# Kernel optimization log

Hardware: AMD Instinct MI355X
Metric: run time of the kernel (lower is better)

Reference implementation:

```python
import jax, jax.numpy as jnp
import numpy as np
from jax import lax

N_LAYERS = 4
D_MODEL = 256
D_INNER = 512   # expand * d_model
D_STATE = 16
D_CONV = 4
DT_RANK = 16    # ceil(d_model/16)
N_FEATURES = 32
N_CLASSES = 3
BATCH, SEQ = 8, 2048


def _layernorm(x, w, b, eps=1e-5):
    mu = x.mean(-1, keepdims=True)
    var = ((x - mu) ** 2).mean(-1, keepdims=True)
    return (x - mu) * lax.rsqrt(var + eps) * w + b


def _silu(x):
    return x * jax.nn.sigmoid(x)


def _ssm(xc, xpW, dtW, dtB, A_log, D):
    # xc: (B,S,d_inner)
    xd = xc @ xpW                                    # (B,S,dt_rank+2*d_state)
    dt_r = xd[..., :DT_RANK]
    Bm = xd[..., DT_RANK:DT_RANK + D_STATE]          # (B,S,N)
    Cm = xd[..., DT_RANK + D_STATE:]                 # (B,S,N)
    dt = jax.nn.softplus(dt_r @ dtW + dtB)           # (B,S,d_inner)
    A = -jnp.exp(A_log)                              # (d_inner,N)
    dA = jnp.exp(dt[..., None] * A)                  # (B,S,d_inner,N)
    dBx = dt[..., None] * Bm[:, :, None, :] * xc[..., None]  # (B,S,d_inner,N)

    def step(h, inp):
        dA_t, dBx_t, C_t = inp                       # (B,d_inner,N),(B,d_inner,N),(B,N)
        h = dA_t * h + dBx_t
        y_t = (h * C_t[:, None, :]).sum(-1)          # (B,d_inner)
        return h, y_t

    h0 = jnp.zeros((xc.shape[0], D_INNER, D_STATE), xc.dtype)
    xs = (dA.transpose(1, 0, 2, 3), dBx.transpose(1, 0, 2, 3), Cm.transpose(1, 0, 2))
    _, ys = lax.scan(step, h0, xs)                   # (S,B,d_inner)
    y = ys.transpose(1, 0, 2)
    return y + xc * D


def _mamba_block(x, inW, convW, convB, xpW, dtW, dtB, A_log, D, outW):
    xz = x @ inW                                     # (B,S,2*d_inner)
    xs, z = xz[..., :D_INNER], xz[..., D_INNER:]
    # causal depthwise conv1d (left-pad d_conv-1)
    xp = jnp.pad(xs, ((0, 0), (D_CONV - 1, 0), (0, 0)))
    xc = lax.conv_general_dilated(
        xp, convW, window_strides=(1,), padding='VALID',
        dimension_numbers=('NWC', 'WIO', 'NWC'),
        feature_group_count=D_INNER) + convB
    xc = _silu(xc)
    y = _ssm(xc, xpW, dtW, dtB, A_log, D)
    y = y * _silu(z)
    return y @ outW


def setup_inputs() -> dict:
    key = jax.random.key(0)
    ks = jax.random.split(key, 20)
    s = 0.02
    L = N_LAYERS
    inp = {
        'x': jax.random.normal(ks[0], (BATCH, SEQ, N_FEATURES), jnp.float32),
        'in_w': jax.random.normal(ks[1], (N_FEATURES, D_MODEL), jnp.float32) * s,
        'in_b': jnp.zeros((D_MODEL,), jnp.float32),
        'ln_w': jnp.ones((L, D_MODEL), jnp.float32),
        'ln_b': jnp.zeros((L, D_MODEL), jnp.float32),
        'inW': jax.random.normal(ks[2], (L, D_MODEL, 2 * D_INNER), jnp.float32) * s,
        'convW': jax.random.normal(ks[3], (L, D_CONV, 1, D_INNER), jnp.float32) * s,
        'convB': jnp.zeros((L, D_INNER), jnp.float32),
        'xpW': jax.random.normal(ks[4], (L, D_INNER, DT_RANK + 2 * D_STATE), jnp.float32) * s,
        'dtW': jax.random.uniform(ks[5], (L, DT_RANK, D_INNER), jnp.float32,
                                  -DT_RANK ** -0.5, DT_RANK ** -0.5),
        'A_log': jnp.broadcast_to(jnp.log(jnp.arange(1, D_STATE + 1, dtype=jnp.float32)),
                                  (L, D_INNER, D_STATE)).copy(),
        'D': jnp.ones((L, D_INNER), jnp.float32),
        'outW': jax.random.normal(ks[6], (L, D_INNER, D_MODEL), jnp.float32) * s,
        'fln_w': jnp.ones((D_MODEL,), jnp.float32),
        'fln_b': jnp.zeros((D_MODEL,), jnp.float32),
        'h1W': jax.random.normal(ks[7], (D_MODEL, D_MODEL // 2), jnp.float32) * s,
        'h1b': jnp.zeros((D_MODEL // 2,), jnp.float32),
        'h2W': jax.random.normal(ks[8], (D_MODEL // 2, N_CLASSES), jnp.float32) * s,
        'h2b': jnp.zeros((N_CLASSES,), jnp.float32),
    }
    # dt bias init: inv softplus of dt ~ LogUniform(dt_min, dt_max)
    dt_min, dt_max = 1e-3, 0.1
    u = jax.random.uniform(ks[9], (L, D_INNER), jnp.float32)
    dt = jnp.clip(jnp.exp(u * (np.log(dt_max) - np.log(dt_min)) + np.log(dt_min)), 1e-4)
    inp['dtB'] = dt + jnp.log(-jnp.expm1(-dt))
    return inp


def reference(x, in_w, in_b, ln_w, ln_b, inW, convW, convB, xpW, dtW, dtB,
              A_log, D, outW, fln_w, fln_b, h1W, h1b, h2W, h2b):
    h = x @ in_w + in_b                              # (B,S,d_model); dropout is eval-mode identity
    for i in range(N_LAYERS):
        h = h + _mamba_block(_layernorm(h, ln_w[i], ln_b[i]),
                             inW[i], convW[i], convB[i], xpW[i],
                             dtW[i], dtB[i], A_log[i], D[i], outW[i])
    h = _layernorm(h, fln_w, fln_b)
    last = h[:, -1]                                  # (B,d_model)
    hidden = jax.nn.gelu(last @ h1W + h1b)
    return hidden @ h2W + h2b                        # (B,n_classes)
```

## Files before the change

kernel.cpp:

```cpp
#include <hip/hip_runtime.h>
#include <math.h>

namespace {

constexpr int NL = 4;
constexpr int DM = 256;
constexpr int DI = 512;
constexpr int DS = 16;
constexpr int DR = 16;
constexpr int NF = 32;
constexpr int NB = 8;
constexpr int T  = 2048;
constexpr int ROWS = NB * T;
constexpr int XD = DR + 2 * DS;
constexpr int NC = 64;
constexpr int CL = T / NC;
constexpr int SCN = NB * DI * DS;

constexpr float LOG2E = 1.44269504088896341f;
constexpr float LN2   = 0.69314718055994531f;

typedef __attribute__((ext_vector_type(4))) float f32x4;
typedef __attribute__((ext_vector_type(8))) short bf16x8;
typedef __attribute__((ext_vector_type(4))) short s16x4;

__device__ __forceinline__ float fexp2(float x) { return __builtin_amdgcn_exp2f(x); }
__device__ __forceinline__ float frcp(float x)  { return __builtin_amdgcn_rcpf(x); }
__device__ __forceinline__ float flog2(float x) { return __builtin_amdgcn_logf(x); }

__device__ __forceinline__ float siluf(float x) {
    return x * frcp(1.f + fexp2(-LOG2E * x));
}
__device__ __forceinline__ float softplusf(float x) {
    return fmaxf(x, 0.f) + LN2 * flog2(1.f + fexp2(-LOG2E * fabsf(x)));
}
__device__ __forceinline__ short f2bf(float f) {
    union { float f; unsigned u; } c; c.f = f;
    unsigned r = (c.u + 0x7FFFu + ((c.u >> 16) & 1u)) >> 16;
    return (short)r;
}
__device__ __forceinline__ float bf2f(short s) {
    union { unsigned u; float f; } c; c.u = ((unsigned)(unsigned short)s) << 16;
    return c.f;
}
__device__ __forceinline__ void powers16(float g, float* a) {
    float g2 = g * g, g4 = g2 * g2, g8 = g4 * g4;
    a[0] = g;        a[1] = g2;       a[2] = g * g2;   a[3] = g4;
    a[4] = g * g4;   a[5] = g2 * g4;  a[6] = a[2] * g4; a[7] = g8;
    a[8] = g * g8;   a[9] = g2 * g8;  a[10] = a[2] * g8; a[11] = g4 * g8;
    a[12] = a[4] * g8; a[13] = a[5] * g8; a[14] = a[6] * g8; a[15] = g8 * g8;
}

__global__ void wtrans(const float* __restrict__ src, short* __restrict__ dst,
                       int K, int N, int Npad, int perL_dst)
{
    const int idx = blockIdx.x * 256 + threadIdx.x;
    const int l = idx / perL_dst;
    const int r = idx - l * perL_dst;
    const unsigned n = (unsigned)r / (unsigned)K;
    const unsigned k = (unsigned)r - n * (unsigned)K;
    float v = (n < (unsigned)N) ? src[(size_t)l * K * N + k * N + n] : 0.f;
    dst[idx] = f2bf(v);
}

__global__ void prep_dtWt(const float* __restrict__ dtW, float* __restrict__ dtWt)
{
    const int idx = blockIdx.x * 256 + threadIdx.x;
    const int l = idx / (DI * DR);
    const int r0 = idx - l * (DI * DR);
    const int d = r0 / DR, rr = r0 - d * DR;
    dtWt[idx] = dtW[(size_t)l * DR * DI + rr * DI + d];
}

__global__ void prep_A2(const float* __restrict__ A_log, float* __restrict__ negA2)
{
    const int i = blockIdx.x * 256 + threadIdx.x;
    negA2[i] = -LOG2E * fexp2(LOG2E * A_log[i]);
}

__global__ void cvt_bf16(const float* __restrict__ src, short* __restrict__ dst)
{
    const int i = blockIdx.x * 256 + threadIdx.x;
    dst[i] = f2bf(src[i]);
}

template <int EP, int BM>
__global__ void gemm_mfma(const short* __restrict__ A, const short* __restrict__ Bt,
                          float* __restrict__ C, short* __restrict__ Cs0,
                          short* __restrict__ Cs1, const float* __restrict__ bias,
                          int K, int lda, int ldc, int Ncut, int NXB, int NYB)
{
    constexpr int MF = BM / 32;
    __shared__ short smem[BM * 40 + 64 * 40];
    const int bid = blockIdx.x;
    const int xcd = bid & 7, j = bid >> 3;
    const int by = xcd * (NYB >> 3) + j / NXB;
    const int bx = j - (j / NXB) * NXB;
    const int m0 = by * BM;
    const int n0 = bx * 64;

    const int tid = threadIdx.x;
    const int lane = tid & 63, w = tid >> 6;
    const int wr = w >> 1, wc = w & 1;
    const int lr = lane & 15, lk = lane >> 4;

    f32x4 acc[MF][2] = {};
    for (int k0 = 0; k0 < K; k0 += 32) {
        __syncthreads();
#pragma unroll
        for (int i = 0; i < BM / 64; ++i) {
            int c = tid + i * 256;
            int row = c >> 2, seg = c & 3;
            bf16x8 v = *(const bf16x8*)(A + (size_t)(m0 + row) * lda + k0 + seg * 8);
            *(bf16x8*)(&smem[row * 40 + seg * 8]) = v;
        }
        {
            int row = tid >> 2, seg = tid & 3;
            bf16x8 v = *(const bf16x8*)(Bt + (size_t)(n0 + row) * K + k0 + seg * 8);
            *(bf16x8*)(&smem[BM * 40 + row * 40 + seg * 8]) = v;
        }
        __syncthreads();
        bf16x8 af[MF], bfr[2];
#pragma unroll
        for (int m = 0; m < MF; ++m)
            af[m] = *(const bf16x8*)(&smem[(wr * (BM / 2) + m * 16 + lr) * 40 + lk * 8]);
#pragma unroll
        for (int n = 0; n < 2; ++n)
            bfr[n] = *(const bf16x8*)(&smem[BM * 40 + (wc * 32 + n * 16 + lr) * 40 + lk * 8]);
#pragma unroll
        for (int m = 0; m < MF; ++m)
#pragma unroll
            for (int n = 0; n < 2; ++n)
                acc[m][n] = __builtin_amdgcn_mfma_f32_16x16x32_bf16(af[m], bfr[n], acc[m][n], 0, 0, 0);
    }
#pragma unroll
    for (int m = 0; m < MF; ++m) {
#pragma unroll
        for (int n = 0; n < 2; ++n) {
            const int col = n0 + wc * 32 + n * 16 + lr;
#pragma unroll
            for (int j2 = 0; j2 < 4; ++j2) {
                const int row = m0 + wr * (BM / 2) + m * 16 + lk * 4 + j2;
                const float v = acc[m][n][j2];
                if (EP == 0) {
                    if (col < DI) Cs0[(size_t)row * DI + col] = f2bf(v);
                    else          Cs1[(size_t)row * DI + col - DI] = f2bf(siluf(v));
                } else if (EP == 1) {
                    if (col < Ncut) C[(size_t)row * ldc + col] = v;
                } else if (EP == 2) {
                    C[(size_t)row * ldc + col] += v;
                } else {
                    C[(size_t)row * ldc + col] = v + bias[col];
                }
            }
        }
    }
}

__global__ void layernorm_kernel(const float* __restrict__ x,
                                 const float* __restrict__ w,
                                 const float* __restrict__ b,
                                 short* __restrict__ out)
{
    const int row = blockIdx.x;
    const int t = threadIdx.x;
    const int wid = t >> 6, lane = t & 63;
    __shared__ float red[4];

    float v = x[row * DM + t];
    float s = v;
#pragma unroll
    for (int o = 32; o >= 1; o >>= 1) s += __shfl_xor(s, o);
    if (lane == 0) red[wid] = s;
    __syncthreads();
    float mu = (red[0] + red[1] + red[2] + red[3]) * (1.f / DM);
    __syncthreads();

    float d = v - mu;
    float q = d * d;
#pragma unroll
    for (int o = 32; o >= 1; o >>= 1) q += __shfl_xor(q, o);
    if (lane == 0) red[wid] = q;
    __syncthreads();
    float var = (red[0] + red[1] + red[2] + red[3]) * (1.f / DM);

    out[row * DM + t] = f2bf(d * (1.f / sqrtf(var + 1e-5f)) * w[t] + b[t]);
}

__global__ void conv_silu_kernel(const short* __restrict__ xsb,
                                 const float* __restrict__ W,
                                 const float* __restrict__ Bc,
                                 short* __restrict__ xcb)
{
    const int idx = blockIdx.x * 256 + threadIdx.x;
    const int c4 = idx & (DI / 4 - 1);
    const int bt = idx >> 7;
    const int t = bt & (T - 1);
    const int c = c4 * 4;
    f32x4 acc = *(const f32x4*)(Bc + c);
#pragma unroll
    for (int k = 0; k < 4; ++k) {
        int tt = t + k - 3;
        if (tt >= 0) {
            s16x4 v = *(const s16x4*)(xsb + (size_t)(bt + k - 3) * DI + c);
            f32x4 wv = *(const f32x4*)(W + k * DI + c);
#pragma unroll
            for (int q = 0; q < 4; ++q) acc[q] += bf2f(v[q]) * wv[q];
        }
    }
    s16x4 o;
#pragma unroll
    for (int q = 0; q < 4; ++q) o[q] = f2bf(siluf(acc[q]));
    *(s16x4*)(xcb + (size_t)idx * 4) = o;
}

__global__ void scan_pass1(const float* __restrict__ xd,
                           const short* __restrict__ xcb,
                           const float* __restrict__ negA2,
                           const float* __restrict__ dtWt,
                           const float* __restrict__ dtB,
                           float* __restrict__ S, float* __restrict__ sdtb)
{
    __shared__ float lds[CL][32];
    const int d = blockIdx.x * 256 + threadIdx.x;
    const int c = blockIdx.y;
    const int b = blockIdx.z;
    const int row0 = b * T + c * CL;

    {
        int t = threadIdx.x >> 3, seg = threadIdx.x & 7;
        *(f32x4*)&lds[t][seg * 4] =
            *(const f32x4*)(xd + (size_t)(row0 + t) * XD + seg * 4);
    }
    float A2[DS], h[DS], wcol[DR];
#pragma unroll
    for (int q = 0; q < 4; ++q) {
        *(f32x4*)&A2[q * 4]   = *(const f32x4*)(negA2 + d * DS + q * 4);
        *(f32x4*)&wcol[q * 4] = *(const f32x4*)(dtWt + d * DR + q * 4);
    }
    bool fastb = true;
#pragma unroll
    for (int s = 1; s < DS; ++s)
        fastb = fastb && (fabsf(A2[s] - A2[0] * (float)(s + 1)) <= 1e-4f * fabsf(A2[s]));
    const bool fast = __all(fastb);
#pragma unroll
    for (int s = 0; s < DS; ++s) h[s] = 0.f;
    const float dtBd = dtB[d];
    float sdt = 0.f;
    __syncthreads();

    for (int t = 0; t < CL; ++t) {
        float xcv = bf2f(xcb[(size_t)(row0 + t) * DI + d]);
        float accd = dtBd;
#pragma unroll
        for (int q = 0; q < 4; ++q) {
            f32x4 xr = *(const f32x4*)&lds[t][q * 4];
            accd += xr[0] * wcol[q * 4] + xr[1] * wcol[q * 4 + 1]
                  + xr[2] * wcol[q * 4 + 2] + xr[3] * wcol[q * 4 + 3];
        }
        float dtv = softplusf(accd);
        float dx = dtv * xcv;
        sdt += dtv;
        float a[DS];
        if (fast) powers16(fexp2(dtv * A2[0]), a);
        else {
#pragma unroll
            for (int s = 0; s < DS; ++s) a[s] = fexp2(dtv * A2[s]);
        }
#pragma unroll
        for (int q = 0; q < 4; ++q) {
            f32x4 Bv = *(const f32x4*)&lds[t][16 + q * 4];
#pragma unroll
            for (int s = 0; s < 4; ++s)
                h[q * 4 + s] = a[q * 4 + s] * h[q * 4 + s] + dx * Bv[s];
        }
    }
    const size_t base = (size_t)c * SCN + ((size_t)b * DI + d) * DS;
#pragma unroll
    for (int q = 0; q < 4; ++q)
        *(f32x4*)(S + base + q * 4) = *(f32x4*)&h[q * 4];
    sdtb[c * (NB * DI) + b * DI + d] = sdt;
}

__global__ void scan_combine(float* __restrict__ S, const float* __restrict__ sdtb,
                             const float* __restrict__ negA2)
{
    const int idx3 = blockIdx.x * blockDim.x + threadIdx.x;
    const int bd = idx3 >> 4;
    const float A2c = negA2[(bd & (DI - 1)) * DS + (idx3 & 15)];
    float h = 0.f;
    for (int c = 0; c < NC; ++c) {
        float sc = S[(size_t)c * SCN + idx3];
        float pc = fexp2(A2c * sdtb[c * (NB * DI) + bd]);
        S[(size_t)c * SCN + idx3] = h;
        h = pc * h + sc;
    }
}

__global__ void scan_pass2(const float* __restrict__ xd,
                           const short* __restrict__ xcb,
                           const float* __restrict__ negA2,
                           const float* __restrict__ dtWt,
                           const float* __restrict__ dtB,
                           const float* __restrict__ Dv,
                           const float* __restrict__ H,
                           const short* __restrict__ zgb,
                           short* __restrict__ yb)
{
    __shared__ float lds[CL][48];
    const int d = blockIdx.x * 256 + threadIdx.x;
    const int c = blockIdx.y;
    const int b = blockIdx.z;
    const int row0 = b * T + c * CL;

    for (int c0 = threadIdx.x; c0 < CL * 12; c0 += 256) {
        int t = c0 / 12, seg = c0 - t * 12;
        *(f32x4*)&lds[t][seg * 4] =
            *(const f32x4*)(xd + (size_t)(row0 + t) * XD + seg * 4);
    }
    float A2[DS], h[DS], wcol[DR];
#pragma unroll
    for (int q = 0; q < 4; ++q) {
        *(f32x4*)&A2[q * 4]   = *(const f32x4*)(negA2 + d * DS + q * 4);
        *(f32x4*)&wcol[q * 4] = *(const f32x4*)(dtWt + d * DR + q * 4);
    }
    bool fastb = true;
#pragma unroll
    for (int s = 1; s < DS; ++s)
        fastb = fastb && (fabsf(A2[s] - A2[0] * (float)(s + 1)) <= 1e-4f * fabsf(A2[s]));
    const bool fast = __all(fastb);
    const size_t base = (size_t)c * SCN + ((size_t)b * DI + d) * DS;
#pragma unroll
    for (int q = 0; q < 4; ++q)
        *(f32x4*)&h[q * 4] = *(const f32x4*)(H + base + q * 4);
    const float dtBd = dtB[d];
    const float Dd = Dv[d];
    __syncthreads();

    for (int t = 0; t < CL; ++t) {
        const size_t row = (size_t)(row0 + t);
        float xcv = bf2f(xcb[row * DI + d]);
        float zg  = bf2f(zgb[row * DI + d]);
        float accd = dtBd;
#pragma unroll
        for (int q = 0; q < 4; ++q) {
            f32x4 xr = *(const f32x4*)&lds[t][q * 4];
            accd += xr[0] * wcol[q * 4] + xr[1] * wcol[q * 4 + 1]
                  + xr[2] * wcol[q * 4 + 2] + xr[3] * wcol[q * 4 + 3];
        }
        float dtv = softplusf(accd);
        float dx = dtv * xcv;
        float a[DS];
        if (fast) powers16(fexp2(dtv * A2[0]), a);
        else {
#pragma unroll
            for (int s = 0; s < DS; ++s) a[s] = fexp2(dtv * A2[s]);
        }
        float acc0 = 0.f, acc1 = 0.f, acc2 = 0.f, acc3 = 0.f;
#pragma unroll
        for (int q = 0; q < 4; ++q) {
            f32x4 Bv = *(const f32x4*)&lds[t][16 + q * 4];
            f32x4 Cv = *(const f32x4*)&lds[t][32 + q * 4];
            h[q * 4 + 0] = a[q * 4 + 0] * h[q * 4 + 0] + dx * Bv[0];
            acc0 += h[q * 4 + 0] * Cv[0];
            h[q * 4 + 1] = a[q * 4 + 1] * h[q * 4 + 1] + dx * Bv[1];
            acc1 += h[q * 4 + 1] * Cv[1];
            h[q * 4 + 2] = a[q * 4 + 2] * h[q * 4 + 2] + dx * Bv[2];
            acc2 += h[q * 4 + 2] * Cv[2];
            h[q * 4 + 3] = a[q * 4 + 3] * h[q * 4 + 3] + dx * Bv[3];
            acc3 += h[q * 4 + 3] * Cv[3];
        }
        float yv = (acc0 + acc1) + (acc2 + acc3);
        yb[row * DI + d] = f2bf((yv + xcv * Dd) * zg);
    }
}

__global__ void head_kernel(const float* __restrict__ h,
                            const float* __restrict__ fw, const float* __restrict__ fb,
                            const float* __restrict__ h1W, const float* __restrict__ h1b,
                            const float* __restrict__ h2W, const float* __restrict__ h2b,
                            float* __restrict__ out)
{
    const int bi = blockIdx.x;
    const int t = threadIdx.x;
    const int wid = t >> 6, lane = t & 63;
    __shared__ float red[4];
    __shared__ float ln[DM];
    __shared__ float hid[DM / 2];

    const float* row = h + ((bi + 1) * T - 1) * DM;
    float v = row[t];
    float s = v;
#pragma unroll
    for (int o = 32; o >= 1; o >>= 1) s += __shfl_xor(s, o);
    if (lane == 0) red[wid] = s;
    __syncthreads();
    float mu = (red[0] + red[1] + red[2] + red[3]) * (1.f / DM);
    __syncthreads();
    float d = v - mu;
    float q = d * d;
#pragma unroll
    for (int o = 32; o >= 1; o >>= 1) q += __shfl_xor(q, o);
    if (lane == 0) red[wid] = q;
    __syncthreads();
    float var = (red[0] + red[1] + red[2] + red[3]) * (1.f / DM);
    ln[t] = d * (1.f / sqrtf(var + 1e-5f)) * fw[t] + fb[t];
    __syncthreads();

    if (t < DM / 2) {
        float acc = h1b[t];
        for (int k = 0; k < DM; ++k) acc += ln[k] * h1W[k * (DM / 2) + t];
        float x3 = acc * acc * acc;
        hid[t] = 0.5f * acc * (1.f + tanhf(0.7978845608028654f * (acc + 0.044715f * x3)));
    }
    __syncthreads();
    if (t < 3) {
        float acc = h2b[t];
        for (int k = 0; k < DM / 2; ++k) acc += hid[k] * h2W[k * 3 + t];
        out[bi * 3 + t] = acc;
    }
}

}

extern "C" void kernel_launch(void* const* d_in, const int* in_sizes, int n_in,
                              void* d_out, int out_size, void* d_ws, size_t ws_size,
                              hipStream_t stream)
{
    (void)in_sizes; (void)n_in; (void)out_size; (void)ws_size;
    const float* x     = (const float*)d_in[0];
    const float* in_w  = (const float*)d_in[1];
    const float* in_b  = (const float*)d_in[2];
    const float* ln_w  = (const float*)d_in[3];
    const float* ln_b  = (const float*)d_in[4];
    const float* inW   = (const float*)d_in[5];
    const float* convW = (const float*)d_in[6];
    const float* convB = (const float*)d_in[7];
    const float* xpW   = (const float*)d_in[8];
    const float* dtW   = (const float*)d_in[9];
    const float* A_log = (const float*)d_in[10];
    const float* Dv    = (const float*)d_in[11];
    const float* outW  = (const float*)d_in[12];
    const float* fln_w = (const float*)d_in[13];
    const float* fln_b = (const float*)d_in[14];
    const float* h1W   = (const float*)d_in[15];
    const float* h1b   = (const float*)d_in[16];
    const float* h2W   = (const float*)d_in[17];
    const float* h2b   = (const float*)d_in[18];
    const float* dtB   = (const float*)d_in[19];
    float* out = (float*)d_out;

    float* w = (float*)d_ws;
    float* hbuf  = w;  w += ROWS * DM;
    float* xd    = w;  w += ROWS * XD;
    float* S     = w;  w += (size_t)SCN * NC;
    float* sdtb  = w;  w += NC * NB * DI;
    float* negA2 = w;  w += NL * DI * DS;
    float* dtWt  = w;  w += NL * DI * DR;
    short* xlnb  = (short*)w;
    short* xb    = xlnb + (size_t)ROWS * DM;
    short* xsb   = xb   + (size_t)ROWS * NF;
    short* zgb   = xsb  + (size_t)ROWS * DI;
    short* xcb   = zgb  + (size_t)ROWS * DI;
    short* yb    = xcb  + (size_t)ROWS * DI;
    short* inWt  = yb   + (size_t)ROWS * DI;
    short* xpWt  = inWt + (size_t)NL * 1024 * DM;
    short* outWt = xpWt + (size_t)NL * 64 * DI;
    short* inwT  = outWt + (size_t)NL * DM * DI;

    wtrans<<<NL * 1024 * DM / 256, 256, 0, stream>>>(inW, inWt, DM, 1024, 1024, 1024 * DM);
    wtrans<<<NL * 64 * DI / 256, 256, 0, stream>>>(xpW, xpWt, DI, XD, 64, 64 * DI);
    wtrans<<<NL * DM * DI / 256, 256, 0, stream>>>(outW, outWt, DI, DM, DM, DM * DI);
    wtrans<<<DM * NF / 256, 256, 0, stream>>>(in_w, inwT, NF, DM, DM, DM * NF);
    prep_dtWt<<<NL * DI * DR / 256, 256, 0, stream>>>(dtW, dtWt);
    prep_A2<<<NL * DI * DS / 256, 256, 0, stream>>>(A_log, negA2);
    cvt_bf16<<<ROWS * NF / 256, 256, 0, stream>>>(x, xb);

    gemm_mfma<3, 128><<<(DM / 64) * (ROWS / 128), 256, 0, stream>>>(
        xb, inwT, hbuf, nullptr, nullptr, in_b, NF, NF, DM, 0, DM / 64, ROWS / 128);

    for (int i = 0; i < NL; ++i) {
        layernorm_kernel<<<ROWS, DM, 0, stream>>>(hbuf, ln_w + i * DM, ln_b + i * DM, xlnb);

        gemm_mfma<0, 128><<<(1024 / 64) * (ROWS / 128), 256, 0, stream>>>(
            xlnb, inWt + (size_t)i * 1024 * DM, nullptr, xsb, zgb, nullptr,
            DM, DM, 0, 0, 1024 / 64, ROWS / 128);

        conv_silu_kernel<<<ROWS * DI / 1024, 256, 0, stream>>>(
            xsb, convW + i * 4 * DI, convB + i * DI, xcb);

        gemm_mfma<1, 64><<<1 * (ROWS / 64), 256, 0, stream>>>(
            xcb, xpWt + (size_t)i * 64 * DI, xd, nullptr, nullptr, nullptr,
            DI, DI, XD, XD, 1, ROWS / 64);

        scan_pass1<<<dim3(DI / 256, NC, NB), 256, 0, stream>>>(
            xd, xcb, negA2 + i * DI * DS, dtWt + i * DI * DR, dtB + i * DI, S, sdtb);
        scan_combine<<<SCN / 256, 256, 0, stream>>>(S, sdtb, negA2 + i * DI * DS);
        scan_pass2<<<dim3(DI / 256, NC, NB), 256, 0, stream>>>(
            xd, xcb, negA2 + i * DI * DS, dtWt + i * DI * DR, dtB + i * DI,
            Dv + i * DI, S, zgb, yb);

        gemm_mfma<2, 128><<<(DM / 64) * (ROWS / 128), 256, 0, stream>>>(
            yb, outWt + (size_t)i * DM * DI, hbuf, nullptr, nullptr, nullptr,
            DI, DI, DM, 0, DM / 64, ROWS / 128);
    }

    head_kernel<<<NB, DM, 0, stream>>>(hbuf, fln_w, fln_b, h1W, h1b, h2W, h2b, out);
}
```

Baseline: 612.3 us.

## Fuse causal conv+SiLU into x_proj GEMM load and scan passes; merge prep kernels

Removes the standalone conv_silu kernel and the xcb intermediate buffer. The depthwise causal conv and SiLU are now recomputed on the fly: in the x_proj GEMM's A-tile load (four shifted row loads per element) and in both scan passes, using a rolling window of three previous inputs. The seven weight-prep launches are also merged into one prep_all kernel. This cuts a full write and read of a bf16 ROWS×DI tensor per layer and several launches. The cost is redundant conv math, extra global loads in the GEMM tile loader, and recomputation in both scan passes.

```diff
diff --git a/kernel.cpp b/kernel.cpp
--- a/kernel.cpp
+++ b/kernel.cpp
@@ -22,7 +22,6 @@
 
 typedef __attribute__((ext_vector_type(4))) float f32x4;
 typedef __attribute__((ext_vector_type(8))) short bf16x8;
-typedef __attribute__((ext_vector_type(4))) short s16x4;
 
 __device__ __forceinline__ float fexp2(float x) { return __builtin_amdgcn_exp2f(x); }
 __device__ __forceinline__ float frcp(float x)  { return __builtin_amdgcn_rcpf(x); }
@@ -51,43 +50,72 @@
     a[12] = a[4] * g8; a[13] = a[5] * g8; a[14] = a[6] * g8; a[15] = g8 * g8;
 }
 
-__global__ void wtrans(const float* __restrict__ src, short* __restrict__ dst,
-                       int K, int N, int Npad, int perL_dst)
-{
-    const int idx = blockIdx.x * 256 + threadIdx.x;
-    const int l = idx / perL_dst;
-    const int r = idx - l * perL_dst;
-    const unsigned n = (unsigned)r / (unsigned)K;
-    const unsigned k = (unsigned)r - n * (unsigned)K;
-    float v = (n < (unsigned)N) ? src[(size_t)l * K * N + k * N + n] : 0.f;
-    dst[idx] = f2bf(v);
-}
-
-__global__ void prep_dtWt(const float* __restrict__ dtW, float* __restrict__ dtWt)
-{
-    const int idx = blockIdx.x * 256 + threadIdx.x;
-    const int l = idx / (DI * DR);
-    const int r0 = idx - l * (DI * DR);
-    const int d = r0 / DR, rr = r0 - d * DR;
-    dtWt[idx] = dtW[(size_t)l * DR * DI + rr * DI + d];
-}
-
-__global__ void prep_A2(const float* __restrict__ A_log, float* __restrict__ negA2)
-{
-    const int i = blockIdx.x * 256 + threadIdx.x;
-    negA2[i] = -LOG2E * fexp2(LOG2E * A_log[i]);
-}
-
-__global__ void cvt_bf16(const float* __restrict__ src, short* __restrict__ dst)
-{
-    const int i = blockIdx.x * 256 + threadIdx.x;
-    dst[i] = f2bf(src[i]);
-}
-
-template <int EP, int BM>
+constexpr int PN1 = NL * 1024 * DM;
+constexpr int PN2 = NL * 64 * DI;
+constexpr int PN3 = NL * DM * DI;
+constexpr int PN4 = DM * NF;
+constexpr int PN5 = NL * DI * DR;
+constexpr int PN6 = NL * DI * DS;
+constexpr int PN7 = ROWS * NF;
+constexpr int PTOT = PN1 + PN2 + PN3 + PN4 + PN5 + PN6 + PN7;
+
+__global__ void prep_all(const float* __restrict__ inW, const float* __restrict__ xpW,
+                         const float* __restrict__ outW, const float* __restrict__ in_w,
+                         const float* __restrict__ dtW, const float* __restrict__ A_log,
+                         const float* __restrict__ x,
+                         short* __restrict__ inWt, short* __restrict__ xpWt,
+                         short* __restrict__ outWt, short* __restrict__ inwT,
+                         float* __restrict__ dtWt, float* __restrict__ negA2,
+                         short* __restrict__ xb)
+{
+    int idx = blockIdx.x * 256 + threadIdx.x;
+    if (idx < PN1) {
+        int l = idx / (1024 * DM), r = idx - l * (1024 * DM);
+        int n = r / DM, k = r - n * DM;
+        inWt[idx] = f2bf(inW[(size_t)l * DM * 1024 + (size_t)k * 1024 + n]);
+        return;
+    }
+    idx -= PN1;
+    if (idx < PN2) {
+        int l = idx / (64 * DI), r = idx - l * (64 * DI);
+        int n = r / DI, k = r - n * DI;
+        xpWt[idx + 0] = (n < XD) ? f2bf(xpW[(size_t)l * DI * XD + (size_t)k * XD + n]) : (short)0;
+        return;
+    }
+    idx -= PN2;
+    if (idx < PN3) {
+        int l = idx / (DM * DI), r = idx - l * (DM * DI);
+        int n = r / DI, k = r - n * DI;
+        outWt[idx] = f2bf(outW[(size_t)l * DI * DM + (size_t)k * DM + n]);
+        return;
+    }
+    idx -= PN3;
+    if (idx < PN4) {
+        int n = idx / NF, k = idx - n * NF;
+        inwT[idx] = f2bf(in_w[(size_t)k * DM + n]);
+        return;
+    }
+    idx -= PN4;
+    if (idx < PN5) {
+        int l = idx / (DI * DR), r0 = idx - l * (DI * DR);
+        int d = r0 / DR, rr = r0 - d * DR;
+        dtWt[idx] = dtW[(size_t)l * DR * DI + (size_t)rr * DI + d];
+        return;
+    }
+    idx -= PN5;
+    if (idx < PN6) {
+        negA2[idx] = -LOG2E * fexp2(LOG2E * A_log[idx]);
+        return;
+    }
+    idx -= PN6;
+    if (idx < PN7) xb[idx] = f2bf(x[idx]);
+}
+
+template <int EP, int BM, int CONVA>
 __global__ void gemm_mfma(const short* __restrict__ A, const short* __restrict__ Bt,
                           float* __restrict__ C, short* __restrict__ Cs0,
                           short* __restrict__ Cs1, const float* __restrict__ bias,
+                          const float* __restrict__ cW, const float* __restrict__ cB,
                           int K, int lda, int ldc, int Ncut, int NXB, int NYB)
 {
     constexpr int MF = BM / 32;
@@ -111,8 +139,30 @@
         for (int i = 0; i < BM / 64; ++i) {
             int c = tid + i * 256;
             int row = c >> 2, seg = c & 3;
-            bf16x8 v = *(const bf16x8*)(A + (size_t)(m0 + row) * lda + k0 + seg * 8);
-            *(bf16x8*)(&smem[row * 40 + seg * 8]) = v;
+            if (CONVA) {
+                const int g = m0 + row;
+                const int t = g & (T - 1);
+                const int ch = k0 + seg * 8;
+                bf16x8 v0 = *(const bf16x8*)(A + (size_t)g * lda + ch);
+                bf16x8 v1{}, v2{}, v3{};
+                if (t >= 1) v1 = *(const bf16x8*)(A + (size_t)(g - 1) * lda + ch);
+                if (t >= 2) v2 = *(const bf16x8*)(A + (size_t)(g - 2) * lda + ch);
+                if (t >= 3) v3 = *(const bf16x8*)(A + (size_t)(g - 3) * lda + ch);
+                bf16x8 o;
+#pragma unroll
+                for (int q = 0; q < 8; ++q) {
+                    float a = cB[ch + q]
+                            + cW[0 * DI + ch + q] * bf2f(v3[q])
+                            + cW[1 * DI + ch + q] * bf2f(v2[q])
+                            + cW[2 * DI + ch + q] * bf2f(v1[q])
+                            + cW[3 * DI + ch + q] * bf2f(v0[q]);
+                    o[q] = f2bf(siluf(a));
+                }
+                *(bf16x8*)(&smem[row * 40 + seg * 8]) = o;
+            } else {
+                bf16x8 v = *(const bf16x8*)(A + (size_t)(m0 + row) * lda + k0 + seg * 8);
+                *(bf16x8*)(&smem[row * 40 + seg * 8]) = v;
+            }
         }
         {
             int row = tid >> 2, seg = tid & 3;
@@ -187,35 +237,10 @@
     out[row * DM + t] = f2bf(d * (1.f / sqrtf(var + 1e-5f)) * w[t] + b[t]);
 }
 
-__global__ void conv_silu_kernel(const short* __restrict__ xsb,
-                                 const float* __restrict__ W,
-                                 const float* __restrict__ Bc,
-                                 short* __restrict__ xcb)
-{
-    const int idx = blockIdx.x * 256 + threadIdx.x;
-    const int c4 = idx & (DI / 4 - 1);
-    const int bt = idx >> 7;
-    const int t = bt & (T - 1);
-    const int c = c4 * 4;
-    f32x4 acc = *(const f32x4*)(Bc + c);
-#pragma unroll
-    for (int k = 0; k < 4; ++k) {
-        int tt = t + k - 3;
-        if (tt >= 0) {
-            s16x4 v = *(const s16x4*)(xsb + (size_t)(bt + k - 3) * DI + c);
-            f32x4 wv = *(const f32x4*)(W + k * DI + c);
-#pragma unroll
-            for (int q = 0; q < 4; ++q) acc[q] += bf2f(v[q]) * wv[q];
-        }
-    }
-    s16x4 o;
-#pragma unroll
-    for (int q = 0; q < 4; ++q) o[q] = f2bf(siluf(acc[q]));
-    *(s16x4*)(xcb + (size_t)idx * 4) = o;
-}
-
 __global__ void scan_pass1(const float* __restrict__ xd,
-                           const short* __restrict__ xcb,
+                           const short* __restrict__ xsb,
+                           const float* __restrict__ cW,
+                           const float* __restrict__ cB,
                            const float* __restrict__ negA2,
                            const float* __restrict__ dtWt,
                            const float* __restrict__ dtB,
@@ -246,11 +271,21 @@
 #pragma unroll
     for (int s = 0; s < DS; ++s) h[s] = 0.f;
     const float dtBd = dtB[d];
+    const float cw0 = cW[d], cw1 = cW[DI + d], cw2 = cW[2 * DI + d], cw3 = cW[3 * DI + d];
+    const float cb = cB[d];
+    float xm1 = 0.f, xm2 = 0.f, xm3 = 0.f;
+    if (c > 0) {
+        xm1 = bf2f(xsb[(size_t)(row0 - 1) * DI + d]);
+        xm2 = bf2f(xsb[(size_t)(row0 - 2) * DI + d]);
+        xm3 = bf2f(xsb[(size_t)(row0 - 3) * DI + d]);
+    }
     float sdt = 0.f;
     __syncthreads();
 
     for (int t = 0; t < CL; ++t) {
-        float xcv = bf2f(xcb[(size_t)(row0 + t) * DI + d]);
+        float xst = bf2f(xsb[(size_t)(row0 + t) * DI + d]);
+        float xcv = siluf(cb + cw0 * xm3 + cw1 * xm2 + cw2 * xm1 + cw3 * xst);
+        xm3 = xm2; xm2 = xm1; xm1 = xst;
         float accd = dtBd;
 #pragma unroll
         for (int q = 0; q < 4; ++q) {
@@ -298,7 +333,9 @@
 }
 
 __global__ void scan_pass2(const float* __restrict__ xd,
-                           const short* __restrict__ xcb,
+                           const short* __restrict__ xsb,
+                           const float* __restrict__ cW,
+                           const float* __restrict__ cB,
                            const float* __restrict__ negA2,
                            const float* __restrict__ dtWt,
                            const float* __restrict__ dtB,
@@ -335,11 +372,21 @@
         *(f32x4*)&h[q * 4] = *(const f32x4*)(H + base + q * 4);
     const float dtBd = dtB[d];
     const float Dd = Dv[d];
+    const float cw0 = cW[d], cw1 = cW[DI + d], cw2 = cW[2 * DI + d], cw3 = cW[3 * DI + d];
+    const float cb = cB[d];
+    float xm1 = 0.f, xm2 = 0.f, xm3 = 0.f;
+    if (c > 0) {
+        xm1 = bf2f(xsb[(size_t)(row0 - 1) * DI + d]);
+        xm2 = bf2f(xsb[(size_t)(row0 - 2) * DI + d]);
+        xm3 = bf2f(xsb[(size_t)(row0 - 3) * DI + d]);
+    }
     __syncthreads();
 
     for (int t = 0; t < CL; ++t) {
         const size_t row = (size_t)(row0 + t);
-        float xcv = bf2f(xcb[row * DI + d]);
+        float xst = bf2f(xsb[row * DI + d]);
+        float xcv = siluf(cb + cw0 * xm3 + cw1 * xm2 + cw2 * xm1 + cw3 * xst);
+        xm3 = xm2; xm2 = xm1; xm1 = xst;
         float zg  = bf2f(zgb[row * DI + d]);
         float accd = dtBd;
 #pragma unroll
@@ -461,48 +508,43 @@
     short* xb    = xlnb + (size_t)ROWS * DM;
     short* xsb   = xb   + (size_t)ROWS * NF;
     short* zgb   = xsb  + (size_t)ROWS * DI;
-    short* xcb   = zgb  + (size_t)ROWS * DI;
-    short* yb    = xcb  + (size_t)ROWS * DI;
+    short* yb    = zgb  + (size_t)ROWS * DI;
     short* inWt  = yb   + (size_t)ROWS * DI;
     short* xpWt  = inWt + (size_t)NL * 1024 * DM;
     short* outWt = xpWt + (size_t)NL * 64 * DI;
     short* inwT  = outWt + (size_t)NL * DM * DI;
 
-    wtrans<<<NL * 1024 * DM / 256, 256, 0, stream>>>(inW, inWt, DM, 1024, 1024, 1024 * DM);
-    wtrans<<<NL * 64 * DI / 256, 256, 0, stream>>>(xpW, xpWt, DI, XD, 64, 64 * DI);
-    wtrans<<<NL * DM * DI / 256, 256, 0, stream>>>(outW, outWt, DI, DM, DM, DM * DI);
-    wtrans<<<DM * NF / 256, 256, 0, stream>>>(in_w, inwT, NF, DM, DM, DM * NF);
-    prep_dtWt<<<NL * DI * DR / 256, 256, 0, stream>>>(dtW, dtWt);
-    prep_A2<<<NL * DI * DS / 256, 256, 0, stream>>>(A_log, negA2);
-    cvt_bf16<<<ROWS * NF / 256, 256, 0, stream>>>(x, xb);
-
-    gemm_mfma<3, 128><<<(DM / 64) * (ROWS / 128), 256, 0, stream>>>(
-        xb, inwT, hbuf, nullptr, nullptr, in_b, NF, NF, DM, 0, DM / 64, ROWS / 128);
+    prep_all<<<(PTOT + 255) / 256, 256, 0, stream>>>(
+        inW, xpW, outW, in_w, dtW, A_log, x,
+        inWt, xpWt, outWt, inwT, dtWt, negA2, xb);
+
+    gemm_mfma<3, 128, 0><<<(DM / 64) * (ROWS / 128), 256, 0, stream>>>(
+        xb, inwT, hbuf, nullptr, nullptr, in_b, nullptr, nullptr,
+        NF, NF, DM, 0, DM / 64, ROWS / 128);
 
     for (int i = 0; i < NL; ++i) {
         layernorm_kernel<<<ROWS, DM, 0, stream>>>(hbuf, ln_w + i * DM, ln_b + i * DM, xlnb);
 
-        gemm_mfma<0, 128><<<(1024 / 64) * (ROWS / 128), 256, 0, stream>>>(
+        gemm_mfma<0, 128, 0><<<(1024 / 64) * (ROWS / 128), 256, 0, stream>>>(
             xlnb, inWt + (size_t)i * 1024 * DM, nullptr, xsb, zgb, nullptr,
-            DM, DM, 0, 0, 1024 / 64, ROWS / 128);
-
-        conv_silu_kernel<<<ROWS * DI / 1024, 256, 0, stream>>>(
-            xsb, convW + i * 4 * DI, convB + i * DI, xcb);
-
-        gemm_mfma<1, 64><<<1 * (ROWS / 64), 256, 0, stream>>>(
-            xcb, xpWt + (size_t)i * 64 * DI, xd, nullptr, nullptr, nullptr,
-            DI, DI, XD, XD, 1, ROWS / 64);
+            nullptr, nullptr, DM, DM, 0, 0, 1024 / 64, ROWS / 128);
+
+        gemm_mfma<1, 64, 1><<<1 * (ROWS / 64), 256, 0, stream>>>(
+            xsb, xpWt + (size_t)i * 64 * DI, xd, nullptr, nullptr, nullptr,
+            convW + i * 4 * DI, convB + i * DI, DI, DI, XD, XD, 1, ROWS / 64);
 
         scan_pass1<<<dim3(DI / 256, NC, NB), 256, 0, stream>>>(
-            xd, xcb, negA2 + i * DI * DS, dtWt + i * DI * DR, dtB + i * DI, S, sdtb);
+            xd, xsb, convW + i * 4 * DI, convB + i * DI,
+            negA2 + i * DI * DS, dtWt + i * DI * DR, dtB + i * DI, S, sdtb);
         scan_combine<<<SCN / 256, 256, 0, stream>>>(S, sdtb, negA2 + i * DI * DS);
         scan_pass2<<<dim3(DI / 256, NC, NB), 256, 0, stream>>>(
-            xd, xcb, negA2 + i * DI * DS, dtWt + i * DI * DR, dtB + i * DI,
+            xd, xsb, convW + i * 4 * DI, convB + i * DI,
+            negA2 + i * DI * DS, dtWt + i * DI * DR, dtB + i * DI,
             Dv + i * DI, S, zgb, yb);
 
-        gemm_mfma<2, 128><<<(DM / 64) * (ROWS / 128), 256, 0, stream>>>(
+        gemm_mfma<2, 128, 0><<<(DM / 64) * (ROWS / 128), 256, 0, stream>>>(
             yb, outWt + (size_t)i * DM * DI, hbuf, nullptr, nullptr, nullptr,
-            DI, DI, DM, 0, DM / 64, ROWS / 128);
+            nullptr, nullptr, DI, DI, DM, 0, DM / 64, ROWS / 128);
     }
 
     head_kernel<<<NB, DM, 0, stream>>>(hbuf, fln_w, fln_b, h1W, h1b, h2W, h2b, out);
```

Result: slower. 633.5 us (+3.5%).
